# Performance work log

Hardware: AMD Instinct MI355X
Metric: run time of the kernel (lower is better)

The kernel has to match this reference:

```python
import jax, jax.numpy as jnp
import numpy as np

B, L, D = 4, 1024, 768
H, Dh = 12, 64
W_ONE_SIDED = 512


def setup_inputs() -> dict:
    key = jax.random.key(0)
    ks = jax.random.split(key, 14)
    std = 0.02
    def lin(k):
        return jax.random.normal(k, (D, D), jnp.float32) * std
    inp = {
        "hidden_states": jax.random.normal(ks[0], (B, L, D), jnp.float32),
        "Wq": lin(ks[1]), "bq": jnp.zeros((D,), jnp.float32),
        "Wk": lin(ks[2]), "bk": jnp.zeros((D,), jnp.float32),
        "Wv": lin(ks[3]), "bv": jnp.zeros((D,), jnp.float32),
        "Wqg": lin(ks[4]), "bqg": jnp.zeros((D,), jnp.float32),
        "Wkg": lin(ks[5]), "bkg": jnp.zeros((D,), jnp.float32),
        "Wvg": lin(ks[6]), "bvg": jnp.zeros((D,), jnp.float32),
    }
    pos = jnp.arange(L)
    # last 64 positions padded; first 8 tokens are global (CLS-like)
    inp["is_index_masked"] = jnp.broadcast_to(pos >= L - 64, (B, L))
    inp["is_index_global_attn"] = jnp.broadcast_to(pos < 8, (B, L))
    return inp


def _split_heads(x):
    # [B, L, D] -> [B, L, H, Dh]
    return x.reshape(B, L, H, Dh)


def reference(hidden_states, Wq, bq, Wk, bk, Wv, bv, Wqg, bqg, Wkg, bkg, Wvg, bvg,
              is_index_masked, is_index_global_attn):
    scale = 1.0 / np.sqrt(Dh)
    x = hidden_states
    Ql = _split_heads(x @ Wq + bq)
    Kl = _split_heads(x @ Wk + bk)
    Vl = _split_heads(x @ Wv + bv)
    Qg = _split_heads(x @ Wqg + bqg)
    Kg = _split_heads(x @ Wkg + bkg)
    Vg = _split_heads(x @ Wvg + bvg)

    neg_inf = jnp.finfo(x.dtype).min
    not_masked = ~is_index_masked
    not_global = ~is_index_global_attn

    # ---- local branch: doubled-K scores [B,H,L,2L] (first half: global-key
    # columns, second half: banded local-key columns), joint softmax ----
    s = jnp.einsum('bqhd,bkhd->bhqk', Ql, Kl) * scale  # [B,H,L,L]
    idx = jnp.arange(L)
    band = jnp.abs(idx[None, :] - idx[:, None]) <= W_ONE_SIDED  # [L,L]
    global_valid = (is_index_global_attn & not_masked)[:, None, None, :]      # [B,1,1,L]
    local_valid = (band[None, :, :] & (not_masked & not_global)[:, None, :])[:, None, :, :]  # [B,1,L,L]
    s_first = jnp.where(global_valid, s, neg_inf)
    s_second = jnp.where(local_valid, s, neg_inf)
    scores_local = jnp.concatenate([s_first, s_second], axis=-1)  # [B,H,L,2L]
    probs = jax.nn.softmax(scores_local.astype(jnp.float32), axis=-1).astype(x.dtype)
    probs = jnp.where(is_index_masked[:, None, :, None], 0.0, probs)
    # (p1 + p2) @ V  ==  p1 @ V + p2 @ V  since K/V are duplicated
    p_sum = probs[..., :L] + probs[..., L:]
    attn_local = jnp.einsum('bhqk,bkhd->bqhd', p_sum, Vl).reshape(B, L, D)

    # ---- global branch: full attention over global projections ----
    sg = jnp.einsum('bqhd,bkhd->bhqk', Qg, Kg) * scale
    sg = jnp.where(is_index_masked[:, None, None, :], neg_inf, sg)
    pg = jax.nn.softmax(sg.astype(jnp.float32), axis=-1).astype(x.dtype)
    pg = jnp.where(is_index_masked[:, None, :, None], 0.0, pg)
    attn_global = jnp.einsum('bhqk,bkhd->bqhd', pg, Vg).reshape(B, L, D)

    # ---- gated combine: global tokens take the global-attention output ----
    output = jnp.where(is_index_global_attn[:, :, None], attn_global, attn_local)
    return output
```

## Files before the change

kernel.cpp:

```cpp
#include <hip/hip_runtime.h>
#include <stdint.h>
#include <math.h>

#define LSEQ 1024
#define NB 4
#define DM 768
#define NHEAD 12
#define HD 64
#define LVALID 960
#define WIN 512

typedef unsigned short u16;
typedef __attribute__((ext_vector_type(8))) short s16x8;
typedef __attribute__((ext_vector_type(4))) float f32x4;

__device__ __forceinline__ u16 f2bf(float f) {
  union { float f; uint32_t u; } v; v.f = f;
  uint32_t r = v.u + 0x7fffu + ((v.u >> 16) & 1u);
  return (u16)(r >> 16);
}
__device__ __forceinline__ float bf2f(u16 h) {
  union { uint32_t u; float f; } v; v.u = ((uint32_t)h) << 16;
  return v.f;
}
__device__ __forceinline__ int swz8(int row, int chunk) {
  return row * 8 + (chunk ^ (row & 7));
}

__device__ __forceinline__ void gload_lds16(const void* g, void* l) {
  __builtin_amdgcn_global_load_lds(
      (const __attribute__((address_space(1))) unsigned int*)g,
      (__attribute__((address_space(3))) unsigned int*)l, 16, 0, 0);
}

#define BARW()                                  \
  do {                                          \
    asm volatile("" ::: "memory");              \
    __builtin_amdgcn_s_barrier();               \
    asm volatile("" ::: "memory");              \
  } while (0)
#define LGKM0() asm volatile("s_waitcnt lgkmcnt(0)" ::: "memory")
#define VMC6() asm volatile("s_waitcnt vmcnt(6)" ::: "memory")
#define VMC0() asm volatile("s_waitcnt vmcnt(0)" ::: "memory")

struct WPtrs { const float* w[6]; };
struct GemmPtrs { const u16* wt[6]; const float* bias[6]; u16* out[6]; };

__global__ __launch_bounds__(256) void prep(const float* __restrict__ x, u16* __restrict__ xb,
                                            WPtrs P, u16* __restrict__ wtb) {
  int bi = blockIdx.x;
  if (bi >= 864) {
    int i = ((bi - 864) * 256 + threadIdx.x) * 8;
    float4 a = *(const float4*)(x + i);
    float4 bq = *(const float4*)(x + i + 4);
    u16 t[8];
    t[0] = f2bf(a.x); t[1] = f2bf(a.y); t[2] = f2bf(a.z); t[3] = f2bf(a.w);
    t[4] = f2bf(bq.x); t[5] = f2bf(bq.y); t[6] = f2bf(bq.z); t[7] = f2bf(bq.w);
    *(uint4*)(xb + i) = *(uint4*)t;
    return;
  }
  int mat = bi / 144, rem = bi - mat * 144;
  int gx = rem % 12, gy = rem / 12;
  const float* W = P.w[mat];
  u16* Wt = wtb + (size_t)mat * DM * DM;
  __shared__ u16 tile[64][72];
  int k0 = gx * 64, n0 = gy * 64;
  int r4 = threadIdx.x >> 4;
  int c4 = (threadIdx.x & 15) * 4;
#pragma unroll
  for (int it = 0; it < 4; it++) {
    int r = it * 16 + r4;
    float4 v = *(const float4*)(W + (size_t)(k0 + r) * DM + n0 + c4);
    tile[c4 + 0][r] = f2bf(v.x);
    tile[c4 + 1][r] = f2bf(v.y);
    tile[c4 + 2][r] = f2bf(v.z);
    tile[c4 + 3][r] = f2bf(v.w);
  }
  __syncthreads();
  int rw = threadIdx.x >> 3, cw = (threadIdx.x & 7) * 8;
#pragma unroll
  for (int it = 0; it < 2; it++) {
    int r = it * 32 + rw;
    *(uint4*)(Wt + (size_t)(n0 + r) * DM + k0 + cw) = *(uint4*)&tile[r][cw];
  }
}

__global__ __launch_bounds__(512, 2) void gemm6(const u16* __restrict__ Xb, GemmPtrs P) {
  int bid = blockIdx.x;
  int xcd = bid & 7;
  int slot = bid >> 3;
  int mat, xt, yt;
  if (slot < 30) {
    int s = slot >> 1;
    int xl = slot & 1;
    int mm = s / 3;
    mat = (mm < 3) ? mm : mm + 1;
    yt = s - mm * 3;
    xt = xcd * 2 + xl;
  } else {
    int j = xcd + 8 * (slot - 30);
    mat = 3;
    xt = (j / 3) * 4;
    yt = j - (j / 3) * 3;
  }
  int m0 = xt * 256, n0 = yt * 256;

  __shared__ __align__(16) u16 SMEM[65536];
  const u16* Wt = P.wt[mat];
  int tid = threadIdx.x;
  int w = tid >> 6, lane = tid & 63, qd = lane >> 4, l16 = lane & 15;
  int wm = w >> 2, wn = w & 3;
  int cx = l16 & 7;

  f32x4 acc[8][4];
  const f32x4 fz = {0.f, 0.f, 0.f, 0.f};
#pragma unroll
  for (int i = 0; i < 8; i++)
#pragma unroll
    for (int j = 0; j < 4; j++) acc[i][j] = fz;

  int aoff[2][2], boff[2][2];
#pragma unroll
  for (int j = 0; j < 2; j++) {
    int s = j * 512 + tid;
    int row = s >> 3;
    int col = ((s & 7) ^ (row & 7)) * 8;
#pragma unroll
    for (int h = 0; h < 2; h++) {
      aoff[j][h] = (m0 + h * 128 + row) * DM + col;
      boff[j][h] = (n0 + h * 128 + row) * DM + col;
    }
  }

  auto stageA = [&](int t, int h) {
#pragma unroll
    for (int j = 0; j < 2; j++)
      gload_lds16(Xb + (size_t)aoff[j][h] + t * 64,
                  &SMEM[(t & 1) * 32768 + h * 8192 + (j * 512 + w * 64) * 8]);
  };
  auto stageB = [&](int t, int h) {
#pragma unroll
    for (int j = 0; j < 2; j++)
      gload_lds16(Wt + (size_t)boff[j][h] + t * 64,
                  &SMEM[(t & 1) * 32768 + 16384 + h * 8192 + (j * 512 + w * 64) * 8]);
  };

  stageA(0, 0); stageA(0, 1);
  stageB(0, 0); stageB(0, 1);
  stageB(1, 0); stageB(1, 1);
  stageA(1, 0);
  VMC6();
  BARW();

  const int rB = (wn & 1) * 64 + l16;

  auto tile = [&](int u) {
    const int buf = u & 1;
    const u16* Ab = &SMEM[buf * 32768 + wm * 8192];
    const u16* Bb = &SMEM[buf * 32768 + 16384 + (wn >> 1) * 8192];
    s16x8 af[4][2], bfr[4][2];
#pragma unroll
    for (int mi = 0; mi < 4; mi++)
#pragma unroll
      for (int ks = 0; ks < 2; ks++)
        af[mi][ks] = *(const s16x8*)(Ab + (mi * 16 + l16) * 64 + ((ks * 4 + qd) ^ cx) * 8);
#pragma unroll
    for (int ni = 0; ni < 2; ni++)
#pragma unroll
      for (int ks = 0; ks < 2; ks++)
        bfr[ni][ks] = *(const s16x8*)(Bb + (rB + ni * 16) * 64 + ((ks * 4 + qd) ^ cx) * 8);
    if (u <= 10) stageA(u + 1, 1);
    BARW();
    LGKM0();
    __builtin_amdgcn_s_setprio(1);
#pragma unroll
    for (int mi = 0; mi < 4; mi++)
#pragma unroll
      for (int ni = 0; ni < 2; ni++)
#pragma unroll
        for (int ks = 0; ks < 2; ks++)
          acc[mi][ni] = __builtin_amdgcn_mfma_f32_16x16x32_bf16(af[mi][ks], bfr[ni][ks],
                                                                acc[mi][ni], 0, 0, 0);
    __builtin_amdgcn_s_setprio(0);
    BARW();
#pragma unroll
    for (int ni = 2; ni < 4; ni++)
#pragma unroll
      for (int ks = 0; ks < 2; ks++)
        bfr[ni][ks] = *(const s16x8*)(Bb + (rB + ni * 16) * 64 + ((ks * 4 + qd) ^ cx) * 8);
    BARW();
    LGKM0();
    __builtin_amdgcn_s_setprio(1);
#pragma unroll
    for (int mi = 0; mi < 4; mi++)
#pragma unroll
      for (int ni = 2; ni < 4; ni++)
#pragma unroll
        for (int ks = 0; ks < 2; ks++)
          acc[mi][ni] = __builtin_amdgcn_mfma_f32_16x16x32_bf16(af[mi][ks], bfr[ni][ks],
                                                                acc[mi][ni], 0, 0, 0);
    __builtin_amdgcn_s_setprio(0);
    BARW();
#pragma unroll
    for (int mi = 0; mi < 4; mi++)
#pragma unroll
      for (int ks = 0; ks < 2; ks++)
        af[mi][ks] = *(const s16x8*)(Ab + ((mi + 4) * 16 + l16) * 64 + ((ks * 4 + qd) ^ cx) * 8);
    if (u <= 9) stageB(u + 2, 0);
    BARW();
    LGKM0();
    __builtin_amdgcn_s_setprio(1);
#pragma unroll
    for (int mi = 0; mi < 4; mi++)
#pragma unroll
      for (int ni = 0; ni < 2; ni++)
#pragma unroll
        for (int ks = 0; ks < 2; ks++)
          acc[mi + 4][ni] = __builtin_amdgcn_mfma_f32_16x16x32_bf16(af[mi][ks], bfr[ni][ks],
                                                                    acc[mi + 4][ni], 0, 0, 0);
    __builtin_amdgcn_s_setprio(0);
    BARW();
    if (u <= 9) {
      stageB(u + 2, 1);
      stageA(u + 2, 0);
      VMC6();
    } else {
      VMC0();
    }
    BARW();
    __builtin_amdgcn_s_setprio(1);
#pragma unroll
    for (int mi = 0; mi < 4; mi++)
#pragma unroll
      for (int ni = 2; ni < 4; ni++)
#pragma unroll
        for (int ks = 0; ks < 2; ks++)
          acc[mi + 4][ni] = __builtin_amdgcn_mfma_f32_16x16x32_bf16(af[mi][ks], bfr[ni][ks],
                                                                    acc[mi + 4][ni], 0, 0, 0);
    __builtin_amdgcn_s_setprio(0);
    BARW();
  };

  for (int u = 0; u < 12; ++u) tile(u);

  const float* bias = P.bias[mat];
  u16* outp = P.out[mat];
  __syncthreads();
  u16* Cs = &SMEM[0];
#pragma unroll
  for (int ni = 0; ni < 4; ni++) {
    int n = wn * 64 + ni * 16 + l16;
    float bvl = bias[n0 + n];
#pragma unroll
    for (int mi = 0; mi < 8; mi++) {
      int mb = wm * 128 + mi * 16 + qd * 4;
#pragma unroll
      for (int r = 0; r < 4; r++) {
        Cs[(mb + r) * 256 + n] = f2bf(acc[mi][ni][r] + bvl);
      }
    }
  }
  __syncthreads();
#pragma unroll
  for (int it = 0; it < 16; it++) {
    int c = it * 512 + tid;
    int row = c >> 5, col = c & 31;
    *(uint4*)(outp + (size_t)(m0 + row) * DM + n0 + col * 8) = ((const uint4*)Cs)[c];
  }
}

__global__ __launch_bounds__(256) void vt_tr(const u16* __restrict__ Vl, u16* __restrict__ Vt) {
  int bi = blockIdx.x;
  int tt = bi & 15, hb = bi >> 4;
  int h = hb % NHEAD, b = hb / NHEAD;
  __shared__ u16 tile[64][72];
  int t0 = tt * 64;
  int tid = threadIdx.x;
#pragma unroll
  for (int it = 0; it < 2; it++) {
    int u = it * 256 + tid;
    int r = u >> 3, cc = u & 7;
    uint4 v = *(const uint4*)(Vl + (size_t)(b * LSEQ + t0 + r) * DM + h * HD + cc * 8);
    *(uint4*)&tile[r][cc * 8] = v;
  }
  __syncthreads();
#pragma unroll
  for (int it = 0; it < 2; it++) {
    int u = it * 256 + tid;
    int dd = u >> 3, tc = u & 7;
    u16 pk[8];
#pragma unroll
    for (int j = 0; j < 8; j++) pk[j] = tile[tc * 8 + j][dd];
    *(uint4*)(Vt + ((size_t)((b * NHEAD + h) * HD) + dd) * LSEQ + t0 + tc * 8) = *(uint4*)pk;
  }
}

__global__ __launch_bounds__(128) void attn_local(
    const u16* __restrict__ Qb, const u16* __restrict__ Kb,
    const u16* __restrict__ Vt, float* __restrict__ out) {
  int q0 = blockIdx.x * 32, h = blockIdx.y, b = blockIdx.z;
  __shared__ u16 Ks[64 * 64], Vs[64 * 64];
  __shared__ u16 Ps[2][16 * 64];
  int tid = threadIdx.x, w = tid >> 6, lane = tid & 63, qd = lane >> 4, l16 = lane & 15;

  int rowK[4], colK[4];
#pragma unroll
  for (int i = 0; i < 4; i++) {
    int s = (w * 4 + i) * 64 + lane;
    rowK[i] = s >> 3;
    colK[i] = ((s & 7) ^ (rowK[i] & 7)) * 8;
  }

  const u16* qrow = Qb + (size_t)(b * LSEQ + q0 + w * 16 + l16) * DM + h * HD;
  s16x8 af0 = *(const s16x8*)(qrow + qd * 8);
  s16x8 af1 = *(const s16x8*)(qrow + 32 + qd * 8);

  float l_part[4] = {0.f, 0.f, 0.f, 0.f};
  f32x4 aO[4];
  const f32x4 fz = {0.f, 0.f, 0.f, 0.f};
#pragma unroll
  for (int nt = 0; nt < 4; nt++) aO[nt] = fz;

  for (int c = 0; c < 16; c++) {
    int kb = c * 64;
    if (c > 0 && !(kb < LVALID && kb + 63 >= q0 - WIN && kb <= q0 + 31 + WIN)) continue;
    __syncthreads();
#pragma unroll
    for (int i = 0; i < 4; i++) {
      gload_lds16(Kb + (size_t)(b * LSEQ + kb + rowK[i]) * DM + h * HD + colK[i],
                  Ks + (size_t)(w * 4 + i) * 512);
      gload_lds16(Vt + (size_t)((b * NHEAD + h) * HD + rowK[i]) * LSEQ + kb + colK[i],
                  Vs + (size_t)(w * 4 + i) * 512);
    }
    __syncthreads();

    float p[4][4];
#pragma unroll
    for (int nt = 0; nt < 4; nt++) {
      s16x8 bk0 = *(const s16x8*)(Ks + swz8(nt * 16 + l16, qd) * 8);
      s16x8 bk1 = *(const s16x8*)(Ks + swz8(nt * 16 + l16, 4 + qd) * 8);
      f32x4 s = fz;
      s = __builtin_amdgcn_mfma_f32_16x16x32_bf16(af0, bk0, s, 0, 0, 0);
      s = __builtin_amdgcn_mfma_f32_16x16x32_bf16(af1, bk1, s, 0, 0, 0);
      int k = kb + nt * 16 + l16;
#pragma unroll
      for (int r = 0; r < 4; r++) {
        int q = q0 + w * 16 + qd * 4 + r;
        bool valid = (k < 8) || (k < LVALID && (k - q) <= WIN && (q - k) <= WIN);
        float sv = valid ? s[r] * 0.125f : -1e30f;
        p[nt][r] = __expf(sv);
        l_part[r] += p[nt][r];
      }
    }

#pragma unroll
    for (int nt = 0; nt < 4; nt++) {
      int chunk = nt * 2 + (l16 >> 3);
      int within = l16 & 7;
#pragma unroll
      for (int r = 0; r < 4; r++) {
        int qrow2 = qd * 4 + r;
        Ps[w][swz8(qrow2, chunk) * 8 + within] = f2bf(p[nt][r]);
      }
    }

    s16x8 pf0 = *(const s16x8*)(&Ps[w][0] + swz8(l16, qd) * 8);
    s16x8 pf1 = *(const s16x8*)(&Ps[w][0] + swz8(l16, 4 + qd) * 8);
#pragma unroll
    for (int nt = 0; nt < 4; nt++) {
      s16x8 v0 = *(const s16x8*)(Vs + swz8(nt * 16 + l16, qd) * 8);
      s16x8 v1 = *(const s16x8*)(Vs + swz8(nt * 16 + l16, 4 + qd) * 8);
      aO[nt] = __builtin_amdgcn_mfma_f32_16x16x32_bf16(pf0, v0, aO[nt], 0, 0, 0);
      aO[nt] = __builtin_amdgcn_mfma_f32_16x16x32_bf16(pf1, v1, aO[nt], 0, 0, 0);
    }
  }

#pragma unroll
  for (int off = 1; off < 16; off <<= 1)
#pragma unroll
    for (int r = 0; r < 4; r++) l_part[r] += __shfl_xor(l_part[r], off);
  float inv[4];
#pragma unroll
  for (int r = 0; r < 4; r++) inv[r] = 1.0f / l_part[r];
#pragma unroll
  for (int nt = 0; nt < 4; nt++)
#pragma unroll
    for (int r = 0; r < 4; r++) {
      int q = q0 + w * 16 + qd * 4 + r;
      out[(size_t)(b * LSEQ + q) * DM + h * HD + nt * 16 + l16] = aO[nt][r] * inv[r];
    }
}

__global__ __launch_bounds__(256) void attn_global(
    const u16* __restrict__ Qgb, const u16* __restrict__ Kgb,
    const u16* __restrict__ Vgb, float* __restrict__ out) {
  int h = blockIdx.x, b = blockIdx.y;
  __shared__ float p_lds[8][960];
  __shared__ float partial[4][8][64];
  int tid = threadIdx.x, w = tid >> 6, lane = tid & 63, qd = lane >> 4, l16 = lane & 15;

  {
    float4 z = {0.f, 0.f, 0.f, 0.f};
#pragma unroll
    for (int it = 0; it < 4; it++) {
      int idx = it * 256 + tid;
      int r = idx >> 4, cc = idx & 15;
      *(float4*)(out + (size_t)(b * LSEQ + LVALID + r) * DM + h * HD + cc * 4) = z;
    }
  }

  const u16* qbase = Qgb + (size_t)(b * LSEQ + l16) * DM + h * HD;
  s16x8 af0 = *(const s16x8*)(qbase + qd * 8);
  s16x8 af1 = *(const s16x8*)(qbase + 32 + qd * 8);
  const f32x4 fz = {0.f, 0.f, 0.f, 0.f};
#pragma unroll
  for (int t = 0; t < 15; t++) {
    int kb = (w + 4 * t) * 16;
    const u16* kbase = Kgb + (size_t)(b * LSEQ + kb + l16) * DM + h * HD;
    s16x8 bk0 = *(const s16x8*)(kbase + qd * 8);
    s16x8 bk1 = *(const s16x8*)(kbase + 32 + qd * 8);
    f32x4 s = fz;
    s = __builtin_amdgcn_mfma_f32_16x16x32_bf16(af0, bk0, s, 0, 0, 0);
    s = __builtin_amdgcn_mfma_f32_16x16x32_bf16(af1, bk1, s, 0, 0, 0);
    if (qd < 2) {
#pragma unroll
      for (int r = 0; r < 4; r++)
        p_lds[qd * 4 + r][kb + l16] = s[r] * 0.125f;
    }
  }
  __syncthreads();

#pragma unroll
  for (int qi = 0; qi < 2; qi++) {
    int q = w * 2 + qi;
    float m = -1e30f;
#pragma unroll
    for (int ki = 0; ki < 15; ki++) m = fmaxf(m, p_lds[q][ki * 64 + lane]);
#pragma unroll
    for (int off = 1; off < 64; off <<= 1) m = fmaxf(m, __shfl_xor(m, off));
    float e[15], ssum = 0.f;
#pragma unroll
    for (int ki = 0; ki < 15; ki++) {
      e[ki] = __expf(p_lds[q][ki * 64 + lane] - m);
      ssum += e[ki];
    }
#pragma unroll
    for (int off = 1; off < 64; off <<= 1) ssum += __shfl_xor(ssum, off);
    float inv = 1.0f / ssum;
#pragma unroll
    for (int ki = 0; ki < 15; ki++) p_lds[q][ki * 64 + lane] = e[ki] * inv;
  }
  __syncthreads();

  float acc[8] = {0.f, 0.f, 0.f, 0.f, 0.f, 0.f, 0.f, 0.f};
  const u16* vcol = Vgb + (size_t)b * LSEQ * DM + h * HD + lane;
  for (int kg = 0; kg < 60; kg++) {
    int k0 = w * 240 + kg * 4;
    float v0 = bf2f(vcol[(size_t)(k0 + 0) * DM]);
    float v1 = bf2f(vcol[(size_t)(k0 + 1) * DM]);
    float v2 = bf2f(vcol[(size_t)(k0 + 2) * DM]);
    float v3 = bf2f(vcol[(size_t)(k0 + 3) * DM]);
#pragma unroll
    for (int q = 0; q < 8; q++) {
      float4 p4 = *(const float4*)&p_lds[q][k0];
      acc[q] += p4.x * v0 + p4.y * v1 + p4.z * v2 + p4.w * v3;
    }
  }
#pragma unroll
  for (int q = 0; q < 8; q++) partial[w][q][lane] = acc[q];
  __syncthreads();
#pragma unroll
  for (int i = 0; i < 2; i++) {
    int idx = tid + 256 * i;
    int q = idx >> 6, d = idx & 63;
    float sum = partial[0][q][d] + partial[1][q][d] + partial[2][q][d] + partial[3][q][d];
    out[(size_t)(b * LSEQ + q) * DM + h * HD + d] = sum;
  }
}

extern "C" void kernel_launch(void* const* d_in, const int* in_sizes, int n_in,
                              void* d_out, int out_size, void* d_ws, size_t ws_size,
                              hipStream_t stream) {
  const float* x = (const float*)d_in[0];
  float* out = (float*)d_out;
  char* ws = (char*)d_ws;

  const size_t XB_SZ = (size_t)4096 * DM * 2;
  const size_t WT_SZ = (size_t)6 * DM * DM * 2;
  const size_t MAT_SZ = (size_t)4096 * DM;
  u16* Xb = (u16*)ws;
  u16* Wt = (u16*)(ws + XB_SZ);
  u16* QKV = (u16*)(ws + XB_SZ + WT_SZ);
  u16* Vt = (u16*)(ws + XB_SZ + WT_SZ + (size_t)6 * MAT_SZ * 2);

  u16* Ql = QKV + 0 * MAT_SZ;
  u16* Kl = QKV + 1 * MAT_SZ;
  u16* Vl = QKV + 2 * MAT_SZ;
  u16* Qg = QKV + 3 * MAT_SZ;
  u16* Kg = QKV + 4 * MAT_SZ;
  u16* Vg = QKV + 5 * MAT_SZ;

  WPtrs wp;
  wp.w[0] = (const float*)d_in[1];
  wp.w[1] = (const float*)d_in[3];
  wp.w[2] = (const float*)d_in[5];
  wp.w[3] = (const float*)d_in[7];
  wp.w[4] = (const float*)d_in[9];
  wp.w[5] = (const float*)d_in[11];
  prep<<<2400, 256, 0, stream>>>(x, Xb, wp, Wt);

  GemmPtrs gp;
  const int bidx[6] = {2, 4, 6, 8, 10, 12};
  u16* outs[6] = {Ql, Kl, Vl, Qg, Kg, Vg};
  for (int i = 0; i < 6; i++) {
    gp.wt[i] = Wt + (size_t)i * DM * DM;
    gp.bias[i] = (const float*)d_in[bidx[i]];
    gp.out[i] = outs[i];
  }
  gemm6<<<252, 512, 0, stream>>>(Xb, gp);

  vt_tr<<<768, 256, 0, stream>>>(Vl, Vt);

  attn_local<<<dim3(30, 12, 4), 128, 0, stream>>>(Ql, Kl, Vt, out);
  attn_global<<<dim3(12, 4), 256, 0, stream>>>(Qg, Kg, Vg, out);
}
```

Before: 188.2 us.

## Remap local-attention blocks, skip mask math on full tiles, widen global kernel

```diff
diff --git a/kernel.cpp b/kernel.cpp
--- a/kernel.cpp
+++ b/kernel.cpp
@@ -298,7 +298,11 @@
 __global__ __launch_bounds__(128) void attn_local(
     const u16* __restrict__ Qb, const u16* __restrict__ Kb,
     const u16* __restrict__ Vt, float* __restrict__ out) {
-  int q0 = blockIdx.x * 32, h = blockIdx.y, b = blockIdx.z;
+  int bid = blockIdx.x;
+  int wid = (bid & 7) * 180 + (bid >> 3);
+  int q0 = (wid % 30) * 32;
+  int hb = wid / 30;
+  int h = hb % NHEAD, b = hb / NHEAD;
   __shared__ u16 Ks[64 * 64], Vs[64 * 64];
   __shared__ u16 Ps[2][16 * 64];
   int tid = threadIdx.x, w = tid >> 6, lane = tid & 63, qd = lane >> 4, l16 = lane & 15;
@@ -334,6 +338,7 @@
     }
     __syncthreads();
 
+    bool fullvalid = (kb + 63 < LVALID) && (kb + 63 <= q0 + WIN) && (q0 + 31 <= kb + WIN);
     float p[4][4];
 #pragma unroll
     for (int nt = 0; nt < 4; nt++) {
@@ -342,14 +347,22 @@
       f32x4 s = fz;
       s = __builtin_amdgcn_mfma_f32_16x16x32_bf16(af0, bk0, s, 0, 0, 0);
       s = __builtin_amdgcn_mfma_f32_16x16x32_bf16(af1, bk1, s, 0, 0, 0);
-      int k = kb + nt * 16 + l16;
-#pragma unroll
-      for (int r = 0; r < 4; r++) {
-        int q = q0 + w * 16 + qd * 4 + r;
-        bool valid = (k < 8) || (k < LVALID && (k - q) <= WIN && (q - k) <= WIN);
-        float sv = valid ? s[r] * 0.125f : -1e30f;
-        p[nt][r] = __expf(sv);
-        l_part[r] += p[nt][r];
+      if (fullvalid) {
+#pragma unroll
+        for (int r = 0; r < 4; r++) {
+          p[nt][r] = __expf(s[r] * 0.125f);
+          l_part[r] += p[nt][r];
+        }
+      } else {
+        int k = kb + nt * 16 + l16;
+#pragma unroll
+        for (int r = 0; r < 4; r++) {
+          int q = q0 + w * 16 + qd * 4 + r;
+          bool valid = (k < 8) || (k < LVALID && (k - q) <= WIN && (q - k) <= WIN);
+          float sv = valid ? s[r] * 0.125f : -1e30f;
+          p[nt][r] = __expf(sv);
+          l_part[r] += p[nt][r];
+        }
       }
     }
 
@@ -391,22 +404,18 @@
     }
 }
 
-__global__ __launch_bounds__(256) void attn_global(
+__global__ __launch_bounds__(1024) void attn_global(
     const u16* __restrict__ Qgb, const u16* __restrict__ Kgb,
     const u16* __restrict__ Vgb, float* __restrict__ out) {
   int h = blockIdx.x, b = blockIdx.y;
   __shared__ float p_lds[8][960];
-  __shared__ float partial[4][8][64];
+  __shared__ float partial[16][8][64];
   int tid = threadIdx.x, w = tid >> 6, lane = tid & 63, qd = lane >> 4, l16 = lane & 15;
 
   {
     float4 z = {0.f, 0.f, 0.f, 0.f};
-#pragma unroll
-    for (int it = 0; it < 4; it++) {
-      int idx = it * 256 + tid;
-      int r = idx >> 4, cc = idx & 15;
-      *(float4*)(out + (size_t)(b * LSEQ + LVALID + r) * DM + h * HD + cc * 4) = z;
-    }
+    int r = tid >> 4, cc = tid & 15;
+    *(float4*)(out + (size_t)(b * LSEQ + LVALID + r) * DM + h * HD + cc * 4) = z;
   }
 
   const u16* qbase = Qgb + (size_t)(b * LSEQ + l16) * DM + h * HD;
@@ -414,25 +423,27 @@
   s16x8 af1 = *(const s16x8*)(qbase + 32 + qd * 8);
   const f32x4 fz = {0.f, 0.f, 0.f, 0.f};
 #pragma unroll
-  for (int t = 0; t < 15; t++) {
-    int kb = (w + 4 * t) * 16;
-    const u16* kbase = Kgb + (size_t)(b * LSEQ + kb + l16) * DM + h * HD;
-    s16x8 bk0 = *(const s16x8*)(kbase + qd * 8);
-    s16x8 bk1 = *(const s16x8*)(kbase + 32 + qd * 8);
-    f32x4 s = fz;
-    s = __builtin_amdgcn_mfma_f32_16x16x32_bf16(af0, bk0, s, 0, 0, 0);
-    s = __builtin_amdgcn_mfma_f32_16x16x32_bf16(af1, bk1, s, 0, 0, 0);
-    if (qd < 2) {
-#pragma unroll
-      for (int r = 0; r < 4; r++)
-        p_lds[qd * 4 + r][kb + l16] = s[r] * 0.125f;
-    }
-  }
-  __syncthreads();
-
-#pragma unroll
-  for (int qi = 0; qi < 2; qi++) {
-    int q = w * 2 + qi;
+  for (int t = 0; t < 4; t++) {
+    int idx = w + 16 * t;
+    if (idx < 60) {
+      int kb = idx * 16;
+      const u16* kbase = Kgb + (size_t)(b * LSEQ + kb + l16) * DM + h * HD;
+      s16x8 bk0 = *(const s16x8*)(kbase + qd * 8);
+      s16x8 bk1 = *(const s16x8*)(kbase + 32 + qd * 8);
+      f32x4 s = fz;
+      s = __builtin_amdgcn_mfma_f32_16x16x32_bf16(af0, bk0, s, 0, 0, 0);
+      s = __builtin_amdgcn_mfma_f32_16x16x32_bf16(af1, bk1, s, 0, 0, 0);
+      if (qd < 2) {
+#pragma unroll
+        for (int r = 0; r < 4; r++)
+          p_lds[qd * 4 + r][kb + l16] = s[r] * 0.125f;
+      }
+    }
+  }
+  __syncthreads();
+
+  if (w < 8) {
+    int q = w;
     float m = -1e30f;
 #pragma unroll
     for (int ki = 0; ki < 15; ki++) m = fmaxf(m, p_lds[q][ki * 64 + lane]);
@@ -454,8 +465,8 @@
 
   float acc[8] = {0.f, 0.f, 0.f, 0.f, 0.f, 0.f, 0.f, 0.f};
   const u16* vcol = Vgb + (size_t)b * LSEQ * DM + h * HD + lane;
-  for (int kg = 0; kg < 60; kg++) {
-    int k0 = w * 240 + kg * 4;
+  for (int kg = 0; kg < 15; kg++) {
+    int k0 = w * 60 + kg * 4;
     float v0 = bf2f(vcol[(size_t)(k0 + 0) * DM]);
     float v1 = bf2f(vcol[(size_t)(k0 + 1) * DM]);
     float v2 = bf2f(vcol[(size_t)(k0 + 2) * DM]);
@@ -469,11 +480,11 @@
 #pragma unroll
   for (int q = 0; q < 8; q++) partial[w][q][lane] = acc[q];
   __syncthreads();
-#pragma unroll
-  for (int i = 0; i < 2; i++) {
-    int idx = tid + 256 * i;
-    int q = idx >> 6, d = idx & 63;
-    float sum = partial[0][q][d] + partial[1][q][d] + partial[2][q][d] + partial[3][q][d];
+  if (tid < 512) {
+    int q = tid >> 6, d = tid & 63;
+    float sum = 0.f;
+#pragma unroll
+    for (int i = 0; i < 16; i++) sum += partial[i][q][d];
     out[(size_t)(b * LSEQ + q) * DM + h * HD + d] = sum;
   }
 }
@@ -521,6 +532,6 @@
 
   vt_tr<<<768, 256, 0, stream>>>(Vl, Vt);
 
-  attn_local<<<dim3(30, 12, 4), 128, 0, stream>>>(Ql, Kl, Vt, out);
-  attn_global<<<dim3(12, 4), 256, 0, stream>>>(Qg, Kg, Vg, out);
-}
+  attn_local<<<1440, 128, 0, stream>>>(Ql, Kl, Vt, out);
+  attn_global<<<dim3(12, 4), 1024, 0, stream>>>(Qg, Kg, Vg, out);
+}
```

New measurement: 180.2 us. 1.04x faster.
